# Performance work log

Hardware: AMD Instinct MI355X
Metric: run time of the kernel (lower is better)

Reference implementation:

```python
import jax, jax.numpy as jnp
import numpy as np

B, T, INPUT_DIM = 4, 2048, 256
D_MODEL = 512                       # hidden_dim // 2
EXPAND = 2
D_INNER = D_MODEL * EXPAND          # 1024
HEADDIM = 128                       # _pick_headdim(1024)
NHEADS = D_INNER // HEADDIM         # 8
DSTATE = 16
DCONV = 4
NLAYERS = 4
CONV_DIM = D_INNER + 2 * DSTATE            # 1056
D_IN_PROJ = 2 * D_INNER + 2 * DSTATE + NHEADS  # 2088
EPS = 1e-5


def _dir_params(key):
    ks = jax.random.split(key, 5)
    return dict(
        in_w=jax.random.normal(ks[0], (NLAYERS, D_IN_PROJ, D_MODEL)) * 0.02,
        conv_w=jax.random.normal(ks[1], (NLAYERS, CONV_DIM, DCONV)) * 0.1,
        conv_b=jnp.zeros((NLAYERS, CONV_DIM)),
        dt_bias=jnp.log(jnp.expm1(jax.random.uniform(ks[2], (NLAYERS, NHEADS), minval=1e-3, maxval=0.1))),
        A_log=jnp.log(jax.random.uniform(ks[3], (NLAYERS, NHEADS), minval=1.0, maxval=16.0)),
        D=jnp.ones((NLAYERS, NHEADS)),
        rms_w=jnp.ones((NLAYERS, D_INNER)),
        out_w=jax.random.normal(ks[4], (NLAYERS, D_MODEL, D_INNER)) * 0.02,
    )


def setup_inputs():
    key = jax.random.key(0)
    kx, ke, kf, kb = jax.random.split(key, 4)
    inp = {
        "x": jax.random.normal(kx, (B, T, INPUT_DIM), dtype=jnp.float32),
        "embed_w": jax.random.normal(ke, (D_MODEL, INPUT_DIM)) * 0.02,
        "embed_b": jnp.zeros((D_MODEL,)),
        "ln1_w": jnp.ones((D_MODEL,)), "ln1_b": jnp.zeros((D_MODEL,)),
        "lnout_w": jnp.ones((2 * D_MODEL,)), "lnout_b": jnp.zeros((2 * D_MODEL,)),
    }
    for tag, p in (("f", _dir_params(kf)), ("b", _dir_params(kb))):
        for k, v in p.items():
            inp[f"{k}_{tag}"] = v
    return inp


def _silu(x):
    return x * jax.nn.sigmoid(x)


def _layernorm(x, w, b):
    m = jnp.mean(x, -1, keepdims=True)
    v = jnp.mean((x - m) ** 2, -1, keepdims=True)
    return (x - m) * jax.lax.rsqrt(v + EPS) * w + b


def _mamba2(h, in_w, conv_w, conv_b, dt_bias, A_log, Dh, rms_w, out_w):
    """One Mamba2 (SSD) block: in_proj -> causal depthwise conv -> selective scan
    -> gated RMSNorm -> out_proj. Sequential scan is math-equivalent to the
    chunked SSD kernel."""
    Bb, Tt, _ = h.shape
    zxbcdt = jnp.einsum('btd,ed->bte', h, in_w)
    z = zxbcdt[..., :D_INNER]
    xBC = zxbcdt[..., D_INNER:D_INNER + CONV_DIM]
    dt = zxbcdt[..., D_INNER + CONV_DIM:]                      # [B,T,H]
    # causal depthwise conv over time (kernel DCONV), then silu
    xc = jax.lax.conv_general_dilated(
        jnp.transpose(xBC, (0, 2, 1)), conv_w[:, None, :], (1,),
        [(DCONV - 1, 0)], feature_group_count=CONV_DIM)
    xBC = _silu(jnp.transpose(xc, (0, 2, 1)) + conv_b)
    xs = xBC[..., :D_INNER].reshape(Bb, Tt, NHEADS, HEADDIM)   # [B,T,H,P]
    Bm = xBC[..., D_INNER:D_INNER + DSTATE]                    # [B,T,N]
    Cm = xBC[..., D_INNER + DSTATE:]                           # [B,T,N]
    dt = jax.nn.softplus(dt + dt_bias)                         # [B,T,H]
    dA = jnp.exp(dt * (-jnp.exp(A_log)))                       # [B,T,H]
    xdt = xs * dt[..., None]                                   # [B,T,H,P]
    tm = lambda a: jnp.moveaxis(a, 1, 0)                       # time-major

    def step(s, inp):
        dA_t, xdt_t, B_t, C_t = inp
        s = dA_t[:, :, None, None] * s + xdt_t[..., None] * B_t[:, None, None, :]
        return s, jnp.einsum('bhpn,bn->bhp', s, C_t)

    s0 = jnp.zeros((Bb, NHEADS, HEADDIM, DSTATE), h.dtype)
    _, ys = jax.lax.scan(step, s0, (tm(dA), tm(xdt), tm(Bm), tm(Cm)))
    y = jnp.moveaxis(ys, 0, 1) + Dh[None, None, :, None] * xs
    y = y.reshape(Bb, Tt, D_INNER)
    g = y * _silu(z)                                           # gated RMSNorm (norm after gate)
    g = g * jax.lax.rsqrt(jnp.mean(g * g, -1, keepdims=True) + EPS) * rms_w
    return jnp.einsum('bti,oi->bto', g, out_w)


def _forward(x, embed_w, embed_b, ln1_w, ln1_b, lnout_w, lnout_b,
             in_w_f, conv_w_f, conv_b_f, dt_bias_f, A_log_f, D_f, rms_w_f, out_w_f,
             in_w_b, conv_w_b, conv_b_b, dt_bias_b, A_log_b, D_b, rms_w_b, out_w_b):
    h = _layernorm(jnp.einsum('bti,oi->bto', x, embed_w) + embed_b, ln1_w, ln1_b)
    h_f, h_b = h, h[:, ::-1]
    for i in range(NLAYERS):
        h_f = _mamba2(h_f, in_w_f[i], conv_w_f[i], conv_b_f[i], dt_bias_f[i],
                      A_log_f[i], D_f[i], rms_w_f[i], out_w_f[i]) + h_f
    for i in range(NLAYERS):
        h_b = _mamba2(h_b, in_w_b[i], conv_w_b[i], conv_b_b[i], dt_bias_b[i],
                      A_log_b[i], D_b[i], rms_w_b[i], out_w_b[i]) + h_b
    out = jnp.concatenate([h_f, h_b[:, ::-1]], axis=-1)        # [B,T,2*D_MODEL]
    return _layernorm(out, lnout_w, lnout_b)


def reference(x, embed_w, embed_b, ln1_w, ln1_b, lnout_w, lnout_b,
              in_w_f, conv_w_f, conv_b_f, dt_bias_f, A_log_f, D_f, rms_w_f, out_w_f,
              in_w_b, conv_w_b, conv_b_b, dt_bias_b, A_log_b, D_b, rms_w_b, out_w_b):
    return _forward(x, embed_w, embed_b, ln1_w, ln1_b, lnout_w, lnout_b,
                    in_w_f, conv_w_f, conv_b_f, dt_bias_f, A_log_f, D_f, rms_w_f, out_w_f,
                    in_w_b, conv_w_b, conv_b_b, dt_bias_b, A_log_b, D_b, rms_w_b, out_w_b)
```

## Files before the change

### kernel.cpp

```cpp
#include <hip/hip_runtime.h>
#include <hip/hip_bf16.h>
#include <math.h>

#define BB 4
#define TT 2048
#define BT 8192
#define DM 512
#define DI 1024
#define NH 8
#define HD 128
#define DS 16
#define CONVD 1056
#define DPROJ 2088
#define NL 4
#define NE 131072

typedef __hip_bfloat16 bf16;
typedef __attribute__((ext_vector_type(8))) short short8;
typedef __attribute__((ext_vector_type(4))) short short4v;
typedef __attribute__((ext_vector_type(4))) float f32x4;

#define AS_G __attribute__((address_space(1)))
#define AS_L __attribute__((address_space(3)))

static __device__ __forceinline__ float b2f_raw(short v){
  union { unsigned u; float f; } c; c.u = ((unsigned)(unsigned short)v) << 16; return c.f;
}
static __device__ __forceinline__ float u32_lo(unsigned u){
  union { unsigned u; float f; } c; c.u = u << 16; return c.f;
}
static __device__ __forceinline__ float u32_hi(unsigned u){
  union { unsigned u; float f; } c; c.u = u & 0xffff0000u; return c.f;
}
static __device__ __forceinline__ unsigned pack_bf16x2(float a, float b){
  unsigned lo = __bfloat16_as_ushort(__float2bfloat16(a));
  unsigned hi = __bfloat16_as_ushort(__float2bfloat16(b));
  return lo | (hi << 16);
}

static __device__ __forceinline__ void red2(float& a, float& b, float* sb){
  #pragma unroll
  for (int o = 32; o; o >>= 1){ a += __shfl_down(a, o); b += __shfl_down(b, o); }
  int w = threadIdx.x >> 6;
  if ((threadIdx.x & 63) == 0){ sb[w] = a; sb[4+w] = b; }
  __syncthreads();
  a = sb[0]+sb[1]+sb[2]+sb[3];
  b = sb[4]+sb[5]+sb[6]+sb[7];
}

__global__ __launch_bounds__(256) void detect_dtype(const void* x, int* flagp){
  __shared__ int cnt;
  if (threadIdx.x == 0) cnt = 0;
  __syncthreads();
  const bf16* p = (const bf16*)x;
  int bad = 0;
  for (int i = threadIdx.x; i < 32768; i += 256){
    float v = __bfloat162float(p[i]);
    if (!isfinite(v) || fabsf(v) > 1e4f) bad++;
  }
  atomicAdd(&cnt, bad);
  __syncthreads();
  if (threadIdx.x == 0) *flagp = (cnt > 100) ? 1 : 0;
}

__global__ __launch_bounds__(256) void convert_in(const void* src, bf16* dst, int n,
                                                  const int* flagp){
  int f = *flagp;
  for (int i = blockIdx.x*256 + threadIdx.x; i < n; i += gridDim.x*256){
    if (f) dst[i] = __float2bfloat16(((const float*)src)[i]);
    else   dst[i] = ((const bf16*)src)[i];
  }
}

template<int OP>
__global__ __launch_bounds__(256,4) void gemm_nt(
    const bf16* __restrict__ A, const bf16* __restrict__ W0, const bf16* __restrict__ W1,
    bf16* C, const bf16* X, float* aux,
    int M, int N, int K, int lda, long sA, long sC)
{
  const int z = blockIdx.z;
  const bf16* Az = A + (long)z * sA;
  const bf16* W = z ? W1 : W0;
  const int m0 = blockIdx.x * 128, n0 = blockIdx.y * 128;
  __shared__ __align__(16) bf16 As[2][128*32];
  __shared__ __align__(16) bf16 Bs[2][128*32];
  const int tid  = threadIdx.x;
  const int lane = tid & 63, wv = tid >> 6;
  const int wmB = (wv >> 1)*64;
  const int wnB = (wv & 1)*64;
  const int quad = lane >> 4, l16 = lane & 15;
  const int srow = lane >> 2;
  const int skb  = (((lane & 3) ^ ((srow >> 1) & 3)) * 16);
  const int rslot = ((quad ^ ((l16 >> 1) & 3)) * 16);

  f32x4 acc[4][4];
  #pragma unroll
  for (int i=0;i<4;i++)
    #pragma unroll
    for (int j=0;j<4;j++) acc[i][j] = (f32x4){0.f,0.f,0.f,0.f};

  auto stage = [&](int k0, int buf){
    #pragma unroll
    for (int is = 0; is < 2; ++is){
      int r = is*64 + wv*16 + srow;
      const char* gA = (const char*)(Az + (long)(m0 + r)*lda + k0) + skb;
      char* lA = (char*)(&As[buf][0]) + (long)(is*64 + wv*16)*64;
      __builtin_amdgcn_global_load_lds((const AS_G void*)gA, (AS_L void*)lA, 16, 0, 0);
    }
    #pragma unroll
    for (int is = 0; is < 2; ++is){
      int r = is*64 + wv*16 + srow;
      int rn = n0 + r; rn = rn < N ? rn : N-1;
      const char* gB = (const char*)(W + (long)rn*K + k0) + skb;
      char* lB = (char*)(&Bs[buf][0]) + (long)(is*64 + wv*16)*64;
      __builtin_amdgcn_global_load_lds((const AS_G void*)gB, (AS_L void*)lB, 16, 0, 0);
    }
  };
  auto compute = [&](int buf){
    short8 af[4], bfr[4];
    #pragma unroll
    for (int mi=0;mi<4;mi++)
      af[mi]  = *(const short8*)((const char*)&As[buf][0] + (long)(wmB+mi*16+l16)*64 + rslot);
    #pragma unroll
    for (int ni=0;ni<4;ni++)
      bfr[ni] = *(const short8*)((const char*)&Bs[buf][0] + (long)(wnB+ni*16+l16)*64 + rslot);
    #pragma unroll
    for (int mi=0;mi<4;mi++)
      #pragma unroll
      for (int ni=0;ni<4;ni++)
        acc[mi][ni] = __builtin_amdgcn_mfma_f32_16x16x32_bf16(af[mi], bfr[ni], acc[mi][ni], 0, 0, 0);
  };

  stage(0, 0);
  __syncthreads();
  for (int k0 = 0; k0 < K; k0 += 64){
    if (k0 + 32 < K) stage(k0 + 32, 1);
    compute(0);
    __syncthreads();
    if (k0 + 64 < K) stage(k0 + 64, 0);
    compute(1);
    __syncthreads();
  }

  bf16* Cz = C + (long)z * sC;
  const bf16* Xz = (OP==2 || OP==4) ? (X + (long)z * sC) : X;
  #pragma unroll
  for (int mi=0;mi<4;mi++){
    #pragma unroll
    for (int ni=0;ni<4;ni++){
      #pragma unroll
      for (int r=0;r<4;r++){
        int row = m0 + wmB + mi*16 + quad*4 + r;
        int col = n0 + wnB + ni*16 + l16;
        if (col < N){
          float v = acc[mi][ni][r];
          if (OP==1) v += __bfloat162float(X[col]);
          if (OP==2) v += __bfloat162float(Xz[(long)row*N + col]);
          if (OP==4){
            v *= aux[(long)z*BT + row];
            v += __bfloat162float(Xz[(long)row*N + col]);
          }
          Cz[(long)row*N + col] = __float2bfloat16(v);
          if (OP==3 && col >= DPROJ-8)
            aux[(long)z*BT*8 + (long)row*8 + (col-(DPROJ-8))] = v;
        }
      }
    }
  }
}

__global__ __launch_bounds__(256) void embed_ln(const bf16* __restrict__ hp,
    const bf16* __restrict__ w, const bf16* __restrict__ bb, bf16* __restrict__ h)
{
  __shared__ float sb[8];
  int bt = blockIdx.x; int b = bt >> 11, t = bt & 2047;
  const bf16* r = hp + (long)bt*DM;
  int c0 = threadIdx.x, c1 = threadIdx.x + 256;
  float v0 = __bfloat162float(r[c0]);
  float v1 = __bfloat162float(r[c1]);
  float s = v0+v1, ss = v0*v0+v1*v1;
  red2(s, ss, sb);
  float m = s / DM;
  float var = ss / DM - m*m;
  float rs = rsqrtf(fmaxf(var, 0.f) + 1e-5f);
  float a0 = (v0-m)*rs*__bfloat162float(w[c0]) + __bfloat162float(bb[c0]);
  float a1 = (v1-m)*rs*__bfloat162float(w[c1]) + __bfloat162float(bb[c1]);
  bf16* o0 = h + (long)bt*DM;
  bf16* o1 = h + ((long)BT + (long)b*TT + (TT-1-t)) * DM;
  o0[c0] = __float2bfloat16(a0); o0[c1] = __float2bfloat16(a1);
  o1[c0] = __float2bfloat16(a0); o1[c1] = __float2bfloat16(a1);
}

__global__ __launch_bounds__(256) void conv_silu(const bf16* __restrict__ zx,
    const bf16* __restrict__ cw0, const bf16* __restrict__ cw1,
    const bf16* __restrict__ cb0, const bf16* __restrict__ cb1,
    bf16* __restrict__ xbc)
{
  int bt = blockIdx.x, dir = blockIdx.y;
  int t = bt & 2047;
  const bf16* cw = dir ? cw1 : cw0;
  const bf16* cb = dir ? cb1 : cb0;
  const bf16* zr = zx + ((long)dir*BT + bt)*DPROJ + DI;
  bf16* orow = xbc + ((long)dir*BT + bt)*CONVD;
  for (int cg = threadIdx.x; cg < CONVD/4; cg += 256){
    int c = cg*4;
    short8 w01 = *(const short8*)(cw + c*4);
    short8 w23 = *(const short8*)(cw + c*4 + 8);
    short4v bi = *(const short4v*)(cb + c);
    float acc[4];
    #pragma unroll
    for (int k=0;k<4;k++) acc[k] = b2f_raw(bi[k]);
    #pragma unroll
    for (int j=0;j<4;j++){
      if (t - 3 + j >= 0){
        short4v xv = *(const short4v*)(zr + (long)(j-3)*DPROJ + c);
        acc[0] = fmaf(b2f_raw(w01[j]),   b2f_raw(xv[0]), acc[0]);
        acc[1] = fmaf(b2f_raw(w01[4+j]), b2f_raw(xv[1]), acc[1]);
        acc[2] = fmaf(b2f_raw(w23[j]),   b2f_raw(xv[2]), acc[2]);
        acc[3] = fmaf(b2f_raw(w23[4+j]), b2f_raw(xv[3]), acc[3]);
      }
    }
    short4v ov;
    #pragma unroll
    for (int k=0;k<4;k++){
      float sg = 1.f / (1.f + expf(-acc[k]));
      ov[k] = (short)__bfloat16_as_ushort(__float2bfloat16(acc[k] * sg));
    }
    *(short4v*)(orow + c) = ov;
  }
}

__global__ __launch_bounds__(256) void dt_kernel(const float* __restrict__ draw,
    const bf16* __restrict__ db0, const bf16* __restrict__ db1,
    const bf16* __restrict__ al0, const bf16* __restrict__ al1,
    float2* __restrict__ dadt)
{
  int idx = blockIdx.x*256 + threadIdx.x;
  int dir = idx >> 16, r = idx & 65535;
  int bt = r >> 3, h = r & 7;
  int b = bt >> 11, t = bt & 2047;
  float x = draw[idx] + __bfloat162float((dir?db1:db0)[h]);
  float sp = (x > 20.f) ? x : log1pf(expf(x));
  float a = expf(-expf(__bfloat162float((dir?al1:al0)[h])) * sp);
  long o = (((long)dir*BB + b)*NH + h)*TT + t;
  float2 v; v.x = a; v.y = sp;
  dadt[o] = v;
}

#define CLG_LOAD(G, T0) do{ \
  _Pragma("unroll") \
  for (int _i=0;_i<4;_i++){ \
    const bf16* _rr = xr + (long)((T0)+_i)*CONVD; \
    G##x[_i]  = *(const unsigned*)(_rr + xoff); \
    G##B0[_i] = *(const short8*)(_rr + DI); \
    G##B1[_i] = *(const short8*)(_rr + DI + 8); \
    G##d[_i]  = ddr[(T0)+_i]; \
  } }while(0)

#define CLG_STEP(G) do{ \
  _Pragma("unroll") \
  for (int _i=0;_i<4;_i++){ \
    float _da = G##d[_i].x, _dt = G##d[_i].y; \
    float _x0 = u32_lo(G##x[_i]), _x1 = u32_hi(G##x[_i]); \
    float _xd0 = _x0*_dt, _xd1 = _x1*_dt; \
    _Pragma("unroll") \
    for (int _n=0;_n<8;_n++){ \
      float _b = b2f_raw(G##B0[_i][_n]); \
      s0[_n] = fmaf(_da, s0[_n], _xd0*_b); \
      s1[_n] = fmaf(_da, s1[_n], _xd1*_b); \
      float _b2 = b2f_raw(G##B1[_i][_n]); \
      s0[8+_n] = fmaf(_da, s0[8+_n], _xd0*_b2); \
      s1[8+_n] = fmaf(_da, s1[8+_n], _xd1*_b2); \
    } \
    pacc *= _da; \
  } }while(0)

__global__ __launch_bounds__(256,1) void chunk_local(const bf16* __restrict__ xbc,
    const float2* __restrict__ dadt, float* __restrict__ SC, float* __restrict__ Pc,
    int cl, int nch)
{
  int c = blockIdx.x;
  int dbh = blockIdx.y*4 + (threadIdx.x >> 6);
  int lane = threadIdx.x & 63;
  int dir = dbh >> 5, b = (dbh >> 3) & 3, h = dbh & 7;
  const bf16* xr = xbc + ((long)dir*BT + (long)b*TT) * CONVD;
  const float2* ddr = dadt + (long)dbh*TT;
  const int xoff = h*HD + lane*2;
  float s0[16], s1[16];
  #pragma unroll
  for (int n=0;n<16;n++){ s0[n]=0.f; s1[n]=0.f; }
  float pacc = 1.f;
  const int c0 = c*cl;

  unsigned Ax[4], Bx[4]; short8 AB0[4], AB1[4], BB0[4], BB1[4]; float2 Ad[4], Bd[4];
  CLG_LOAD(A, c0);
  for (int t0 = c0; t0 < c0+cl; t0 += 8){
    CLG_LOAD(B, t0+4);
    CLG_STEP(A);
    if (t0+8 < c0+cl) CLG_LOAD(A, t0+8);
    CLG_STEP(B);
  }
  float* sc = SC + (long)c*NE + (long)dbh*2048 + lane*32;
  #pragma unroll
  for (int n=0;n<16;n++){ sc[n] = s0[n]; sc[16+n] = s1[n]; }
  if (lane == 0) Pc[dbh*nch + c] = pacc;
}

template<int NCH>
__global__ __launch_bounds__(256) void chunk_combine(float* __restrict__ SC,
    const float* __restrict__ Pc)
{
  int e = blockIdx.x*256 + threadIdx.x;
  int dbh = e >> 11;
  float s = 0.f;
  #pragma unroll
  for (int c=0;c<NCH;c++){
    float tmp = SC[(long)c*NE + e];
    SC[(long)c*NE + e] = s;
    s = Pc[dbh*NCH + c]*s + tmp;
  }
}

__global__ __launch_bounds__(512,2) void chunk_apply_gate(
    const bf16* __restrict__ xbc, bf16* __restrict__ zx,
    const float2* __restrict__ dadt, const float* __restrict__ SC,
    const bf16* __restrict__ D0, const bf16* __restrict__ D1,
    const bf16* __restrict__ rw0, const bf16* __restrict__ rw1,
    float* __restrict__ psum, int cl)
{
  int c = blockIdx.x;
  int db = blockIdx.y;
  int dir = db >> 2, b = db & 3;
  int h = threadIdx.x >> 6;
  int lane = threadIdx.x & 63;
  int dbh = dir*32 + b*8 + h;
  const bf16* xr = xbc + ((long)dir*BT + (long)b*TT) * CONVD;
  bf16* zrow = zx + ((long)dir*BT + (long)b*TT) * DPROJ;
  const long rowB = (long)dir*BT + (long)b*TT;
  const float2* ddr = dadt + (long)dbh*TT;
  const int xoff = h*HD + lane*2;
  float Dv = __bfloat162float(dir ? D1[h] : D0[h]);
  const bf16* rw = dir ? rw1 : rw0;
  float rwl = __bfloat162float(rw[xoff]);
  float rwh = __bfloat162float(rw[xoff+1]);
  const float* sc = SC + (long)c*NE + (long)dbh*2048 + lane*32;
  float s0[16], s1[16];
  #pragma unroll
  for (int n=0;n<16;n++){ s0[n] = sc[n]; s1[n] = sc[16+n]; }
  const int c0 = c*cl;

  for (int t0 = c0; t0 < c0+cl; t0 += 4){
    float gl[4], gh[4], sum2[4];
    #pragma unroll
    for (int i=0;i<4;i++){
      const bf16* rr = xr + (long)(t0+i)*CONVD;
      unsigned xv = *(const unsigned*)(rr + xoff);
      short8 B0 = *(const short8*)(rr + DI);
      short8 B1 = *(const short8*)(rr + DI + 8);
      short8 C0 = *(const short8*)(rr + DI + DS);
      short8 C1 = *(const short8*)(rr + DI + DS + 8);
      unsigned zv = *(const unsigned*)(zrow + (long)(t0+i)*DPROJ + xoff);
      float2 dd = ddr[t0+i];
      float da = dd.x, dt = dd.y;
      float x0 = u32_lo(xv), x1 = u32_hi(xv);
      float xd0 = x0*dt, xd1 = x1*dt;
      float a0 = 0.f, a1 = 0.f;
      #pragma unroll
      for (int n=0;n<8;n++){
        float bb0 = b2f_raw(B0[n]), cc0 = b2f_raw(C0[n]);
        s0[n] = fmaf(da, s0[n], xd0*bb0);
        s1[n] = fmaf(da, s1[n], xd1*bb0);
        a0 = fmaf(s0[n], cc0, a0);
        a1 = fmaf(s1[n], cc0, a1);
        float bb1 = b2f_raw(B1[n]), cc1 = b2f_raw(C1[n]);
        s0[8+n] = fmaf(da, s0[8+n], xd0*bb1);
        s1[8+n] = fmaf(da, s1[8+n], xd1*bb1);
        a0 = fmaf(s0[8+n], cc1, a0);
        a1 = fmaf(s1[8+n], cc1, a1);
      }
      float y0 = a0 + Dv*x0, y1 = a1 + Dv*x1;
      float z0 = u32_lo(zv), z1 = u32_hi(zv);
      float g0 = y0 * z0 * (1.f/(1.f+expf(-z0)));
      float g1 = y1 * z1 * (1.f/(1.f+expf(-z1)));
      sum2[i] = g0*g0 + g1*g1;
      gl[i] = g0*rwl; gh[i] = g1*rwh;
    }
    #pragma unroll
    for (int o=32;o;o>>=1){
      #pragma unroll
      for (int i=0;i<4;i++) sum2[i] += __shfl_down(sum2[i], o);
    }
    if (lane == 0){
      #pragma unroll
      for (int i=0;i<4;i++) psum[(rowB + t0 + i)*8 + h] = sum2[i];
    }
    #pragma unroll
    for (int i=0;i<4;i++)
      *(unsigned*)(zrow + (long)(t0+i)*DPROJ + xoff) = pack_bf16x2(gl[i], gh[i]);
  }
}

__global__ __launch_bounds__(256) void rms_scl(const float* __restrict__ psum,
                                               float* __restrict__ scl)
{
  int r = blockIdx.x*256 + threadIdx.x;
  float s = 0.f;
  #pragma unroll
  for (int w=0;w<8;w++) s += psum[(long)r*8 + w];
  scl[r] = rsqrtf(s*(1.f/DI) + 1e-5f);
}

__global__ __launch_bounds__(256) void final_ln(const bf16* __restrict__ h,
    const bf16* __restrict__ lw, const bf16* __restrict__ lb, void* out,
    int mode, const int* flagp)
{
  __shared__ float sb[8];
  int bt = blockIdx.x; int b = bt >> 11, t = bt & 2047;
  int f32out = mode ? *flagp : 0;
  const bf16* rf = h + (long)bt*DM;
  const bf16* rb = h + ((long)BT + (long)b*TT + (TT-1-t))*DM;
  float v[4], s = 0.f, ss = 0.f;
  #pragma unroll
  for (int i=0;i<4;i++){
    int c = threadIdx.x + i*256;
    v[i] = __bfloat162float(c < DM ? rf[c] : rb[c-DM]);
    s += v[i]; ss += v[i]*v[i];
  }
  red2(s, ss, sb);
  float m = s / (2*DM);
  float var = ss / (2*DM) - m*m;
  float rs = rsqrtf(fmaxf(var, 0.f) + 1e-5f);
  #pragma unroll
  for (int i=0;i<4;i++){
    int c = threadIdx.x + i*256;
    float o = (v[i]-m)*rs*__bfloat162float(lw[c]) + __bfloat162float(lb[c]);
    if (f32out) ((float*)out)[(long)bt*(2*DM) + c] = o;
    else        ((bf16*)out)[(long)bt*(2*DM) + c] = __float2bfloat16(o);
  }
}

extern "C" void kernel_launch(void* const* d_in, const int* in_sizes, int n_in,
                              void* d_out, int out_size, void* d_ws, size_t ws_size,
                              hipStream_t stream)
{
  char* wsp = (char*)d_ws;
  auto take = [&](size_t bytes){ char* p = wsp; wsp += (bytes + 63) & ~(size_t)63; return p; };
  int*   flagp = (int*)  take(4);
  bf16*  h     = (bf16*) take((size_t)2*BT*DM*2);
  bf16*  zx    = (bf16*) take((size_t)2*BT*DPROJ*2);
  bf16*  xbc   = (bf16*) take((size_t)2*BT*CONVD*2);
  float2* dadt = (float2*)take((size_t)2*BB*NH*TT*8);
  float* draw  = (float*)take((size_t)2*BT*NH*4);
  float* Pc    = (float*)take((size_t)64*64*4);
  float* psum  = (float*)take((size_t)2*BT*8*4);
  float* scl   = (float*)take((size_t)2*BT*4);
  char* preCanon = wsp;

  static const int cnt[23] = {
    BT*256, DM*256, DM, DM, DM, 2*DM, 2*DM,
    NL*DPROJ*DM, NL*CONVD*4, NL*CONVD, NL*NH, NL*NH, NL*NH, NL*DI, NL*DM*DI,
    NL*DPROJ*DM, NL*CONVD*4, NL*CONVD, NL*NH, NL*NH, NL*NH, NL*DI, NL*DM*DI };
  bf16* canon[23];
  for (int i = 0; i < 23; ++i) canon[i] = (bf16*)take((size_t)cnt[i]*2);
  char* postCanon = wsp;

  const size_t scUnit = (size_t)NE*4;
  size_t usedFull   = (size_t)(postCanon - (char*)d_ws);
  size_t usedDirect = (size_t)(preCanon  - (char*)d_ws);
  int convMode, NCHR; float* SC;
  if      (ws_size >= usedFull + 64*scUnit){ convMode=1; NCHR=64; SC=(float*)postCanon; }
  else if (ws_size >= usedFull + 32*scUnit){ convMode=1; NCHR=32; SC=(float*)postCanon; }
  else if (ws_size >= usedFull + 16*scUnit){ convMode=1; NCHR=16; SC=(float*)postCanon; }
  else {
    convMode = 0;
    if      (ws_size >= usedDirect + 64*scUnit) NCHR=64;
    else if (ws_size >= usedDirect + 32*scUnit) NCHR=32;
    else                                        NCHR=16;
    SC = (float*)preCanon;
  }
  const int CLR = TT / NCHR;

  const bf16* in[23];
  if (convMode){
    detect_dtype<<<1,256,0,stream>>>(d_in[0], flagp);
    for (int i = 0; i < 23; ++i){
      int grid = (cnt[i] + 255)/256; if (grid > 2048) grid = 2048;
      convert_in<<<grid,256,0,stream>>>(d_in[i], canon[i], cnt[i], flagp);
      in[i] = canon[i];
    }
  } else {
    for (int i = 0; i < 23; ++i) in[i] = (const bf16*)d_in[i];
  }

  const bf16* x       = in[0];
  const bf16* embed_w = in[1];
  const bf16* embed_b = in[2];
  const bf16* ln1_w   = in[3];
  const bf16* ln1_b   = in[4];
  const bf16* lnout_w = in[5];
  const bf16* lnout_b = in[6];
  const bf16* in_w[2]   = {in[7],  in[15]};
  const bf16* conv_w[2] = {in[8],  in[16]};
  const bf16* conv_b[2] = {in[9],  in[17]};
  const bf16* dt_b[2]   = {in[10], in[18]};
  const bf16* A_log[2]  = {in[11], in[19]};
  const bf16* Dp[2]     = {in[12], in[20]};
  const bf16* rms_w[2]  = {in[13], in[21]};
  const bf16* out_w[2]  = {in[14], in[22]};

  bf16* hpre = xbc;

  gemm_nt<1><<<dim3(64,4,1),256,0,stream>>>(x, embed_w, embed_w, hpre, embed_b, nullptr,
                                            BT, DM, 256, 256, 0, 0);
  embed_ln<<<dim3(BT),256,0,stream>>>(hpre, ln1_w, ln1_b, h);

  for (int i = 0; i < NL; ++i){
    gemm_nt<3><<<dim3(64,17,2),256,0,stream>>>(h, in_w[0]+(size_t)i*DPROJ*DM, in_w[1]+(size_t)i*DPROJ*DM,
        zx, nullptr, draw, BT, DPROJ, DM, DM, (long)BT*DM, (long)BT*DPROJ);
    conv_silu<<<dim3(BT,2),256,0,stream>>>(zx, conv_w[0]+(size_t)i*CONVD*4, conv_w[1]+(size_t)i*CONVD*4,
        conv_b[0]+(size_t)i*CONVD, conv_b[1]+(size_t)i*CONVD, xbc);
    dt_kernel<<<dim3(512),256,0,stream>>>(draw, dt_b[0]+i*NH, dt_b[1]+i*NH,
        A_log[0]+i*NH, A_log[1]+i*NH, dadt);
    chunk_local<<<dim3(NCHR,16),256,0,stream>>>(xbc, dadt, SC, Pc, CLR, NCHR);
    if      (NCHR == 64) chunk_combine<64><<<dim3(NE/256),256,0,stream>>>(SC, Pc);
    else if (NCHR == 32) chunk_combine<32><<<dim3(NE/256),256,0,stream>>>(SC, Pc);
    else                 chunk_combine<16><<<dim3(NE/256),256,0,stream>>>(SC, Pc);
    chunk_apply_gate<<<dim3(NCHR,8),512,0,stream>>>(xbc, zx, dadt, SC,
        Dp[0]+i*NH, Dp[1]+i*NH, rms_w[0]+(size_t)i*DI, rms_w[1]+(size_t)i*DI, psum, CLR);
    rms_scl<<<dim3(2*BT/256),256,0,stream>>>(psum, scl);
    gemm_nt<4><<<dim3(64,4,2),256,0,stream>>>(zx, out_w[0]+(size_t)i*DM*DI, out_w[1]+(size_t)i*DM*DI,
        h, h, scl, BT, DM, DI, DPROJ, (long)BT*DPROJ, (long)BT*DM);
  }

  final_ln<<<dim3(BT),256,0,stream>>>(h, lnout_w, lnout_b, d_out, convMode, flagp);
  (void)in_sizes; (void)n_in; (void)out_size;
}
```

Baseline: 1.137 ms.

## Fuse causal conv+SiLU for x channels into chunk scan kernels, keep only B/C buffer

```diff
diff --git a/kernel.cpp b/kernel.cpp
--- a/kernel.cpp
+++ b/kernel.cpp
@@ -191,43 +191,43 @@
   o1[c0] = __float2bfloat16(a0); o1[c1] = __float2bfloat16(a1);
 }
 
-__global__ __launch_bounds__(256) void conv_silu(const bf16* __restrict__ zx,
+__global__ __launch_bounds__(256) void conv_bc(const bf16* __restrict__ zx,
     const bf16* __restrict__ cw0, const bf16* __restrict__ cw1,
     const bf16* __restrict__ cb0, const bf16* __restrict__ cb1,
-    bf16* __restrict__ xbc)
-{
-  int bt = blockIdx.x, dir = blockIdx.y;
-  int t = bt & 2047;
+    bf16* __restrict__ BC)
+{
+  int idx = blockIdx.x*256 + threadIdx.x;
+  int dir = idx >> 16;
+  int rem = idx & 65535;
+  int r = rem >> 3, cg = rem & 7;
+  int t = r & 2047;
+  int c = DI + cg*4;
   const bf16* cw = dir ? cw1 : cw0;
   const bf16* cb = dir ? cb1 : cb0;
-  const bf16* zr = zx + ((long)dir*BT + bt)*DPROJ + DI;
-  bf16* orow = xbc + ((long)dir*BT + bt)*CONVD;
-  for (int cg = threadIdx.x; cg < CONVD/4; cg += 256){
-    int c = cg*4;
-    short8 w01 = *(const short8*)(cw + c*4);
-    short8 w23 = *(const short8*)(cw + c*4 + 8);
-    short4v bi = *(const short4v*)(cb + c);
-    float acc[4];
-    #pragma unroll
-    for (int k=0;k<4;k++) acc[k] = b2f_raw(bi[k]);
-    #pragma unroll
-    for (int j=0;j<4;j++){
-      if (t - 3 + j >= 0){
-        short4v xv = *(const short4v*)(zr + (long)(j-3)*DPROJ + c);
-        acc[0] = fmaf(b2f_raw(w01[j]),   b2f_raw(xv[0]), acc[0]);
-        acc[1] = fmaf(b2f_raw(w01[4+j]), b2f_raw(xv[1]), acc[1]);
-        acc[2] = fmaf(b2f_raw(w23[j]),   b2f_raw(xv[2]), acc[2]);
-        acc[3] = fmaf(b2f_raw(w23[4+j]), b2f_raw(xv[3]), acc[3]);
-      }
-    }
-    short4v ov;
-    #pragma unroll
-    for (int k=0;k<4;k++){
-      float sg = 1.f / (1.f + expf(-acc[k]));
-      ov[k] = (short)__bfloat16_as_ushort(__float2bfloat16(acc[k] * sg));
-    }
-    *(short4v*)(orow + c) = ov;
-  }
+  const bf16* zcol = zx + ((long)dir*BT + r)*DPROJ + DI + c;
+  short8 wa = *(const short8*)(cw + c*4);
+  short8 wb = *(const short8*)(cw + c*4 + 8);
+  short4v bi = *(const short4v*)(cb + c);
+  float acc[4];
+  #pragma unroll
+  for (int k=0;k<4;k++) acc[k] = b2f_raw(bi[k]);
+  #pragma unroll
+  for (int j=0;j<4;j++){
+    if (t - 3 + j >= 0){
+      short4v xv = *(const short4v*)(zcol + (long)(j-3)*DPROJ);
+      acc[0] = fmaf(b2f_raw(wa[j]),   b2f_raw(xv[0]), acc[0]);
+      acc[1] = fmaf(b2f_raw(wa[4+j]), b2f_raw(xv[1]), acc[1]);
+      acc[2] = fmaf(b2f_raw(wb[j]),   b2f_raw(xv[2]), acc[2]);
+      acc[3] = fmaf(b2f_raw(wb[4+j]), b2f_raw(xv[3]), acc[3]);
+    }
+  }
+  short4v ov;
+  #pragma unroll
+  for (int k=0;k<4;k++){
+    float sg = 1.f / (1.f + expf(-acc[k]));
+    ov[k] = (short)__bfloat16_as_ushort(__float2bfloat16(acc[k] * sg));
+  }
+  *(short4v*)(BC + ((long)dir*BT + r)*32 + cg*4) = ov;
 }
 
 __global__ __launch_bounds__(256) void dt_kernel(const float* __restrict__ draw,
@@ -247,58 +247,75 @@
   dadt[o] = v;
 }
 
-#define CLG_LOAD(G, T0) do{ \
-  _Pragma("unroll") \
-  for (int _i=0;_i<4;_i++){ \
-    const bf16* _rr = xr + (long)((T0)+_i)*CONVD; \
-    G##x[_i]  = *(const unsigned*)(_rr + xoff); \
-    G##B0[_i] = *(const short8*)(_rr + DI); \
-    G##B1[_i] = *(const short8*)(_rr + DI + 8); \
-    G##d[_i]  = ddr[(T0)+_i]; \
-  } }while(0)
-
-#define CLG_STEP(G) do{ \
-  _Pragma("unroll") \
-  for (int _i=0;_i<4;_i++){ \
-    float _da = G##d[_i].x, _dt = G##d[_i].y; \
-    float _x0 = u32_lo(G##x[_i]), _x1 = u32_hi(G##x[_i]); \
-    float _xd0 = _x0*_dt, _xd1 = _x1*_dt; \
-    _Pragma("unroll") \
-    for (int _n=0;_n<8;_n++){ \
-      float _b = b2f_raw(G##B0[_i][_n]); \
-      s0[_n] = fmaf(_da, s0[_n], _xd0*_b); \
-      s1[_n] = fmaf(_da, s1[_n], _xd1*_b); \
-      float _b2 = b2f_raw(G##B1[_i][_n]); \
-      s0[8+_n] = fmaf(_da, s0[8+_n], _xd0*_b2); \
-      s1[8+_n] = fmaf(_da, s1[8+_n], _xd1*_b2); \
-    } \
-    pacc *= _da; \
-  } }while(0)
-
-__global__ __launch_bounds__(256,1) void chunk_local(const bf16* __restrict__ xbc,
-    const float2* __restrict__ dadt, float* __restrict__ SC, float* __restrict__ Pc,
-    int cl, int nch)
+__global__ __launch_bounds__(256,1) void chunk_local(
+    const bf16* __restrict__ zx, const bf16* __restrict__ BC,
+    const float2* __restrict__ dadt,
+    const bf16* __restrict__ cw0, const bf16* __restrict__ cw1,
+    const bf16* __restrict__ cb0, const bf16* __restrict__ cb1,
+    float* __restrict__ SC, float* __restrict__ Pc, int cl, int nch)
 {
   int c = blockIdx.x;
   int dbh = blockIdx.y*4 + (threadIdx.x >> 6);
   int lane = threadIdx.x & 63;
   int dir = dbh >> 5, b = (dbh >> 3) & 3, h = dbh & 7;
-  const bf16* xr = xbc + ((long)dir*BT + (long)b*TT) * CONVD;
+  const long rowB = (long)dir*BT + (long)b*TT;
+  const int cc = h*HD + lane*2;
+  const bf16* zxr = zx + rowB*DPROJ + DI + cc;
+  const bf16* bcr = BC + rowB*32;
   const float2* ddr = dadt + (long)dbh*TT;
-  const int xoff = h*HD + lane*2;
+  const bf16* cw = dir ? cw1 : cw0;
+  short8 wv = *(const short8*)(cw + cc*4);
+  float w00=b2f_raw(wv[0]),w01=b2f_raw(wv[1]),w02=b2f_raw(wv[2]),w03=b2f_raw(wv[3]);
+  float w10=b2f_raw(wv[4]),w11=b2f_raw(wv[5]),w12=b2f_raw(wv[6]),w13=b2f_raw(wv[7]);
+  unsigned bu = *(const unsigned*)((dir?cb1:cb0) + cc);
+  float bias0 = u32_lo(bu), bias1 = u32_hi(bu);
+
   float s0[16], s1[16];
   #pragma unroll
   for (int n=0;n<16;n++){ s0[n]=0.f; s1[n]=0.f; }
   float pacc = 1.f;
-  const int c0 = c*cl;
-
-  unsigned Ax[4], Bx[4]; short8 AB0[4], AB1[4], BB0[4], BB1[4]; float2 Ad[4], Bd[4];
-  CLG_LOAD(A, c0);
-  for (int t0 = c0; t0 < c0+cl; t0 += 8){
-    CLG_LOAD(B, t0+4);
-    CLG_STEP(A);
-    if (t0+8 < c0+cl) CLG_LOAD(A, t0+8);
-    CLG_STEP(B);
+  const int c0t = c*cl;
+
+  float xm3_0=0.f,xm3_1=0.f,xm2_0=0.f,xm2_1=0.f,xm1_0=0.f,xm1_1=0.f;
+  if (c0t >= 3){
+    unsigned a;
+    a = *(const unsigned*)(zxr + (long)(c0t-3)*DPROJ); xm3_0=u32_lo(a); xm3_1=u32_hi(a);
+    a = *(const unsigned*)(zxr + (long)(c0t-2)*DPROJ); xm2_0=u32_lo(a); xm2_1=u32_hi(a);
+    a = *(const unsigned*)(zxr + (long)(c0t-1)*DPROJ); xm1_0=u32_lo(a); xm1_1=u32_hi(a);
+  }
+
+  for (int t0 = c0t; t0 < c0t+cl; t0 += 4){
+    unsigned xu[4]; short8 B0[4], B1[4]; float2 dd[4];
+    #pragma unroll
+    for (int i=0;i<4;i++){
+      xu[i] = *(const unsigned*)(zxr + (long)(t0+i)*DPROJ);
+      const bf16* bc = bcr + (long)(t0+i)*32;
+      B0[i] = *(const short8*)(bc);
+      B1[i] = *(const short8*)(bc + 8);
+      dd[i] = ddr[t0+i];
+    }
+    #pragma unroll
+    for (int i=0;i<4;i++){
+      float xt0=u32_lo(xu[i]), xt1=u32_hi(xu[i]);
+      float cv0 = fmaf(w03,xt0,fmaf(w02,xm1_0,fmaf(w01,xm2_0,fmaf(w00,xm3_0,bias0))));
+      float cv1 = fmaf(w13,xt1,fmaf(w12,xm1_1,fmaf(w11,xm2_1,fmaf(w10,xm3_1,bias1))));
+      xm3_0=xm2_0; xm2_0=xm1_0; xm1_0=xt0;
+      xm3_1=xm2_1; xm2_1=xm1_1; xm1_1=xt1;
+      float xs0 = cv0 * (1.f/(1.f+expf(-cv0)));
+      float xs1 = cv1 * (1.f/(1.f+expf(-cv1)));
+      float da=dd[i].x, dt=dd[i].y;
+      float xd0=xs0*dt, xd1=xs1*dt;
+      #pragma unroll
+      for (int n=0;n<8;n++){
+        float bb=b2f_raw(B0[i][n]);
+        s0[n]=fmaf(da,s0[n],xd0*bb);
+        s1[n]=fmaf(da,s1[n],xd1*bb);
+        float b2=b2f_raw(B1[i][n]);
+        s0[8+n]=fmaf(da,s0[8+n],xd0*b2);
+        s1[8+n]=fmaf(da,s1[8+n],xd1*b2);
+      }
+      pacc *= da;
+    }
   }
   float* sc = SC + (long)c*NE + (long)dbh*2048 + lane*32;
   #pragma unroll
@@ -322,8 +339,10 @@
 }
 
 __global__ __launch_bounds__(512,2) void chunk_apply_gate(
-    const bf16* __restrict__ xbc, bf16* __restrict__ zx,
+    bf16* __restrict__ zx, const bf16* __restrict__ BC,
     const float2* __restrict__ dadt, const float* __restrict__ SC,
+    const bf16* __restrict__ cw0, const bf16* __restrict__ cw1,
+    const bf16* __restrict__ cb0, const bf16* __restrict__ cb1,
     const bf16* __restrict__ D0, const bf16* __restrict__ D1,
     const bf16* __restrict__ rw0, const bf16* __restrict__ rw1,
     float* __restrict__ psum, int cl)
@@ -334,36 +353,57 @@
   int h = threadIdx.x >> 6;
   int lane = threadIdx.x & 63;
   int dbh = dir*32 + b*8 + h;
-  const bf16* xr = xbc + ((long)dir*BT + (long)b*TT) * CONVD;
-  bf16* zrow = zx + ((long)dir*BT + (long)b*TT) * DPROJ;
   const long rowB = (long)dir*BT + (long)b*TT;
+  const int cc = h*HD + lane*2;
+  const bf16* zxr = zx + rowB*DPROJ + DI + cc;
+  bf16* zrow = zx + rowB*DPROJ;
+  const bf16* bcr = BC + rowB*32;
   const float2* ddr = dadt + (long)dbh*TT;
-  const int xoff = h*HD + lane*2;
+  const bf16* cw = dir ? cw1 : cw0;
+  short8 wv = *(const short8*)(cw + cc*4);
+  float w00=b2f_raw(wv[0]),w01=b2f_raw(wv[1]),w02=b2f_raw(wv[2]),w03=b2f_raw(wv[3]);
+  float w10=b2f_raw(wv[4]),w11=b2f_raw(wv[5]),w12=b2f_raw(wv[6]),w13=b2f_raw(wv[7]);
+  unsigned bu = *(const unsigned*)((dir?cb1:cb0) + cc);
+  float bias0 = u32_lo(bu), bias1 = u32_hi(bu);
   float Dv = __bfloat162float(dir ? D1[h] : D0[h]);
   const bf16* rw = dir ? rw1 : rw0;
-  float rwl = __bfloat162float(rw[xoff]);
-  float rwh = __bfloat162float(rw[xoff+1]);
+  float rwl = __bfloat162float(rw[cc]);
+  float rwh = __bfloat162float(rw[cc+1]);
   const float* sc = SC + (long)c*NE + (long)dbh*2048 + lane*32;
   float s0[16], s1[16];
   #pragma unroll
   for (int n=0;n<16;n++){ s0[n] = sc[n]; s1[n] = sc[16+n]; }
-  const int c0 = c*cl;
-
-  for (int t0 = c0; t0 < c0+cl; t0 += 4){
+  const int c0t = c*cl;
+
+  float xm3_0=0.f,xm3_1=0.f,xm2_0=0.f,xm2_1=0.f,xm1_0=0.f,xm1_1=0.f;
+  if (c0t >= 3){
+    unsigned a;
+    a = *(const unsigned*)(zxr + (long)(c0t-3)*DPROJ); xm3_0=u32_lo(a); xm3_1=u32_hi(a);
+    a = *(const unsigned*)(zxr + (long)(c0t-2)*DPROJ); xm2_0=u32_lo(a); xm2_1=u32_hi(a);
+    a = *(const unsigned*)(zxr + (long)(c0t-1)*DPROJ); xm1_0=u32_lo(a); xm1_1=u32_hi(a);
+  }
+
+  for (int t0 = c0t; t0 < c0t+cl; t0 += 4){
     float gl[4], gh[4], sum2[4];
     #pragma unroll
     for (int i=0;i<4;i++){
-      const bf16* rr = xr + (long)(t0+i)*CONVD;
-      unsigned xv = *(const unsigned*)(rr + xoff);
-      short8 B0 = *(const short8*)(rr + DI);
-      short8 B1 = *(const short8*)(rr + DI + 8);
-      short8 C0 = *(const short8*)(rr + DI + DS);
-      short8 C1 = *(const short8*)(rr + DI + DS + 8);
-      unsigned zv = *(const unsigned*)(zrow + (long)(t0+i)*DPROJ + xoff);
+      unsigned xv = *(const unsigned*)(zxr + (long)(t0+i)*DPROJ);
+      const bf16* bc = bcr + (long)(t0+i)*32;
+      short8 B0 = *(const short8*)(bc);
+      short8 B1 = *(const short8*)(bc + 8);
+      short8 C0 = *(const short8*)(bc + 16);
+      short8 C1 = *(const short8*)(bc + 24);
+      unsigned zv = *(const unsigned*)(zrow + (long)(t0+i)*DPROJ + cc);
       float2 dd = ddr[t0+i];
+      float xt0=u32_lo(xv), xt1=u32_hi(xv);
+      float cv0 = fmaf(w03,xt0,fmaf(w02,xm1_0,fmaf(w01,xm2_0,fmaf(w00,xm3_0,bias0))));
+      float cv1 = fmaf(w13,xt1,fmaf(w12,xm1_1,fmaf(w11,xm2_1,fmaf(w10,xm3_1,bias1))));
+      xm3_0=xm2_0; xm2_0=xm1_0; xm1_0=xt0;
+      xm3_1=xm2_1; xm2_1=xm1_1; xm1_1=xt1;
+      float xs0 = cv0 * (1.f/(1.f+expf(-cv0)));
+      float xs1 = cv1 * (1.f/(1.f+expf(-cv1)));
       float da = dd.x, dt = dd.y;
-      float x0 = u32_lo(xv), x1 = u32_hi(xv);
-      float xd0 = x0*dt, xd1 = x1*dt;
+      float xd0 = xs0*dt, xd1 = xs1*dt;
       float a0 = 0.f, a1 = 0.f;
       #pragma unroll
       for (int n=0;n<8;n++){
@@ -378,7 +418,7 @@
         a0 = fmaf(s0[8+n], cc1, a0);
         a1 = fmaf(s1[8+n], cc1, a1);
       }
-      float y0 = a0 + Dv*x0, y1 = a1 + Dv*x1;
+      float y0 = a0 + Dv*xs0, y1 = a1 + Dv*xs1;
       float z0 = u32_lo(zv), z1 = u32_hi(zv);
       float g0 = y0 * z0 * (1.f/(1.f+expf(-z0)));
       float g1 = y1 * z1 * (1.f/(1.f+expf(-z1)));
@@ -396,7 +436,7 @@
     }
     #pragma unroll
     for (int i=0;i<4;i++)
-      *(unsigned*)(zrow + (long)(t0+i)*DPROJ + xoff) = pack_bf16x2(gl[i], gh[i]);
+      *(unsigned*)(zrow + (long)(t0+i)*DPROJ + cc) = pack_bf16x2(gl[i], gh[i]);
   }
 }
 
@@ -448,7 +488,8 @@
   int*   flagp = (int*)  take(4);
   bf16*  h     = (bf16*) take((size_t)2*BT*DM*2);
   bf16*  zx    = (bf16*) take((size_t)2*BT*DPROJ*2);
-  bf16*  xbc   = (bf16*) take((size_t)2*BT*CONVD*2);
+  bf16*  hpre  = (bf16*) take((size_t)BT*DM*2);
+  bf16*  BCb   = (bf16*) take((size_t)2*BT*32*2);
   float2* dadt = (float2*)take((size_t)2*BB*NH*TT*8);
   float* draw  = (float*)take((size_t)2*BT*NH*4);
   float* Pc    = (float*)take((size_t)64*64*4);
@@ -508,25 +549,26 @@
   const bf16* rms_w[2]  = {in[13], in[21]};
   const bf16* out_w[2]  = {in[14], in[22]};
 
-  bf16* hpre = xbc;
-
   gemm_nt<1><<<dim3(64,4,1),256,0,stream>>>(x, embed_w, embed_w, hpre, embed_b, nullptr,
                                             BT, DM, 256, 256, 0, 0);
   embed_ln<<<dim3(BT),256,0,stream>>>(hpre, ln1_w, ln1_b, h);
 
   for (int i = 0; i < NL; ++i){
+    const bf16* cwl0 = conv_w[0]+(size_t)i*CONVD*4, *cwl1 = conv_w[1]+(size_t)i*CONVD*4;
+    const bf16* cbl0 = conv_b[0]+(size_t)i*CONVD,   *cbl1 = conv_b[1]+(size_t)i*CONVD;
     gemm_nt<3><<<dim3(64,17,2),256,0,stream>>>(h, in_w[0]+(size_t)i*DPROJ*DM, in_w[1]+(size_t)i*DPROJ*DM,
         zx, nullptr, draw, BT, DPROJ, DM, DM, (long)BT*DM, (long)BT*DPROJ);
-    conv_silu<<<dim3(BT,2),256,0,stream>>>(zx, conv_w[0]+(size_t)i*CONVD*4, conv_w[1]+(size_t)i*CONVD*4,
-        conv_b[0]+(size_t)i*CONVD, conv_b[1]+(size_t)i*CONVD, xbc);
+    conv_bc<<<dim3(512),256,0,stream>>>(zx, cwl0, cwl1, cbl0, cbl1, BCb);
     dt_kernel<<<dim3(512),256,0,stream>>>(draw, dt_b[0]+i*NH, dt_b[1]+i*NH,
         A_log[0]+i*NH, A_log[1]+i*NH, dadt);
-    chunk_local<<<dim3(NCHR,16),256,0,stream>>>(xbc, dadt, SC, Pc, CLR, NCHR);
+    chunk_local<<<dim3(NCHR,16),256,0,stream>>>(zx, BCb, dadt, cwl0, cwl1, cbl0, cbl1,
+        SC, Pc, CLR, NCHR);
     if      (NCHR == 64) chunk_combine<64><<<dim3(NE/256),256,0,stream>>>(SC, Pc);
     else if (NCHR == 32) chunk_combine<32><<<dim3(NE/256),256,0,stream>>>(SC, Pc);
     else                 chunk_combine<16><<<dim3(NE/256),256,0,stream>>>(SC, Pc);
-    chunk_apply_gate<<<dim3(NCHR,8),512,0,stream>>>(xbc, zx, dadt, SC,
-        Dp[0]+i*NH, Dp[1]+i*NH, rms_w[0]+(size_t)i*DI, rms_w[1]+(size_t)i*DI, psum, CLR);
+    chunk_apply_gate<<<dim3(NCHR,8),512,0,stream>>>(zx, BCb, dadt, SC,
+        cwl0, cwl1, cbl0, cbl1, Dp[0]+i*NH, Dp[1]+i*NH,
+        rms_w[0]+(size_t)i*DI, rms_w[1]+(size_t)i*DI, psum, CLR);
     rms_scl<<<dim3(2*BT/256),256,0,stream>>>(psum, scl);
     gemm_nt<4><<<dim3(64,4,2),256,0,stream>>>(zx, out_w[0]+(size_t)i*DM*DI, out_w[1]+(size_t)i*DM*DI,
         h, h, scl, BT, DM, DI, DPROJ, (long)BT*DPROJ, (long)BT*DM);
```

After: 1.199 ms. 5.4% more time.
